# Kernel optimization log

Measured on AMD Instinct MI355X. Metric: run time of the kernel, lower is better.

The kernel has to match this reference:

```python
import jax, jax.numpy as jnp
import numpy as np

MROPE_SECTION = [16, 24, 24]
HEAD_DIM = 128
NUM_HEADS = 16
NUM_KV_HEADS = 8
EPS = 1e-6


def rmsnorm(x, w, eps=EPS):
    xf = x.astype(jnp.float32)
    var = jnp.mean(xf * xf, axis=-1, keepdims=True)
    return (w * (xf * jax.lax.rsqrt(var + eps))).astype(x.dtype)


def rotate_half(x):
    d = x.shape[-1] // 2
    return jnp.concatenate([-x[..., d:], x[..., :d]], axis=-1)


def build_mrope(c):
    # c: [3, B, S, head_dim]; pick modality i%3 per section (non-interleaved path)
    sec = MROPE_SECTION * 2
    splits = np.cumsum(sec)[:-1]
    parts = jnp.split(c, splits, axis=-1)
    out = jnp.concatenate([p[i % 3] for i, p in enumerate(parts)], axis=-1)  # [B,S,hd]
    return out[:, None]  # unsqueeze dim 1 -> [B,1,S,hd]


def setup_inputs() -> dict:
    key = jax.random.key(0)
    ks = jax.random.split(key, 8)
    B, S, D = 2, 2048, 2048
    hd, H, KV = HEAD_DIM, NUM_HEADS, NUM_KV_HEADS
    hidden_states = jax.random.normal(ks[0], (B, S, D), jnp.float32)
    cos = jax.random.uniform(ks[1], (3, B, S, hd), jnp.float32, -1.0, 1.0)
    sin = jax.random.uniform(ks[2], (3, B, S, hd), jnp.float32, -1.0, 1.0)
    # additive causal mask [B,1,S,S]
    neg = jnp.full((S, S), -1e9, jnp.float32)
    causal = jnp.triu(neg, k=1)
    attention_mask = jnp.broadcast_to(causal[None, None], (B, 1, S, S))
    sc = 0.02
    Wq = jax.random.normal(ks[3], (D, H * hd), jnp.float32) * sc
    Wk = jax.random.normal(ks[4], (D, KV * hd), jnp.float32) * sc
    Wv = jax.random.normal(ks[5], (D, KV * hd), jnp.float32) * sc
    Wo = jax.random.normal(ks[6], (H * hd, D), jnp.float32) * sc
    q_norm_w = jnp.ones((hd,), jnp.float32)
    k_norm_w = jnp.ones((hd,), jnp.float32)
    return dict(hidden_states=hidden_states, cos=cos, sin=sin,
                attention_mask=attention_mask, Wq=Wq, Wk=Wk, Wv=Wv, Wo=Wo,
                q_norm_w=q_norm_w, k_norm_w=k_norm_w)


def reference(hidden_states, cos, sin, attention_mask, Wq, Wk, Wv, Wo, q_norm_w, k_norm_w):
    B, S, D = hidden_states.shape
    hd, H, KV = HEAD_DIM, NUM_HEADS, NUM_KV_HEADS
    groups = H // KV
    scaling = hd ** -0.5

    q = (hidden_states @ Wq).reshape(B, S, H, hd)
    k = (hidden_states @ Wk).reshape(B, S, KV, hd)
    v = (hidden_states @ Wv).reshape(B, S, KV, hd)

    q = rmsnorm(q, q_norm_w).transpose(0, 2, 1, 3)  # [B,H,S,hd]
    k = rmsnorm(k, k_norm_w).transpose(0, 2, 1, 3)  # [B,KV,S,hd]
    v = v.transpose(0, 2, 1, 3)                      # [B,KV,S,hd]

    c = build_mrope(cos)  # [B,1,S,hd]
    s = build_mrope(sin)
    q = q * c + rotate_half(q) * s
    k = k * c + rotate_half(k) * s

    # repeat_kv (GQA)
    k = jnp.repeat(k, groups, axis=1)  # [B,H,S,hd]
    v = jnp.repeat(v, groups, axis=1)

    scores = jnp.einsum('bhqd,bhkd->bhqk', q, k) * scaling + attention_mask
    attn = jax.nn.softmax(scores.astype(jnp.float32), axis=-1).astype(q.dtype)
    out = jnp.einsum('bhqk,bhkd->bqhd', attn, v).reshape(B, S, H * hd)
    return out @ Wo
```

## Files before the change

### kernel.cpp

```cpp
#include <hip/hip_runtime.h>
#include <hip/hip_bf16.h>

typedef unsigned short u16;
typedef __bf16 bf16x8 __attribute__((ext_vector_type(8)));
typedef float f32x4 __attribute__((ext_vector_type(4)));

#define B_ 2
#define S_ 2048
#define SCALE_LOG2E 0.12751743f

static __device__ __forceinline__ u16 f2bf(float f) {
    union { float f; unsigned int u; } v; v.f = f;
    unsigned int r = v.u + 0x7fffu + ((v.u >> 16) & 1u);
    return (u16)(r >> 16);
}
static __device__ __forceinline__ float bf2f(unsigned int u) {
    union { unsigned int u; float f; } v; v.u = u << 16;
    return v.f;
}

__device__ __forceinline__ void gload16(const u16* g, u16* l) {
    __builtin_amdgcn_global_load_lds(
        (const __attribute__((address_space(1))) u16*)g,
        (__attribute__((address_space(3))) u16*)l,
        16, 0, 0);
}

__global__ __launch_bounds__(256) void prep(
    const float* __restrict__ hs, u16* __restrict__ hsb,
    const float* __restrict__ Wq, const float* __restrict__ Wk,
    const float* __restrict__ Wv, const float* __restrict__ Wo,
    u16* __restrict__ wqkvb, u16* __restrict__ wob)
{
    __shared__ float tile[32][33];
    int z = blockIdx.x;
    if (z < 8192) {
        int i = z * 256 + threadIdx.x;
        float4 v = reinterpret_cast<const float4*>(hs)[i];
        ushort4 o;
        o.x = f2bf(v.x); o.y = f2bf(v.y); o.z = f2bf(v.z); o.w = f2bf(v.w);
        reinterpret_cast<ushort4*>(hsb)[i] = o;
        return;
    }
    z -= 8192;
    const float* src; u16* dst; int srs, ct, zz;
    if (z < 4096)      { src = Wq; dst = wqkvb;               srs = 2048; ct = 64; zz = z; }
    else if (z < 6144) { src = Wk; dst = wqkvb + 2048 * 2048; srs = 1024; ct = 32; zz = z - 4096; }
    else if (z < 8192) { src = Wv; dst = wqkvb + 3072 * 2048; srs = 1024; ct = 32; zz = z - 6144; }
    else               { src = Wo; dst = wob;                 srs = 2048; ct = 64; zz = z - 8192; }
    int c0 = (zz % ct) << 5, r0 = (zz / ct) << 5;
    int t = threadIdx.x, tx = t & 7, ty = t >> 3;
    float4 v = *(const float4*)&src[(size_t)(r0 + ty) * srs + c0 + 4 * tx];
    tile[ty][4 * tx + 0] = v.x; tile[ty][4 * tx + 1] = v.y;
    tile[ty][4 * tx + 2] = v.z; tile[ty][4 * tx + 3] = v.w;
    __syncthreads();
    ushort4 o;
    o.x = f2bf(tile[4 * tx + 0][ty]); o.y = f2bf(tile[4 * tx + 1][ty]);
    o.z = f2bf(tile[4 * tx + 2][ty]); o.w = f2bf(tile[4 * tx + 3][ty]);
    *(ushort4*)&dst[(size_t)(c0 + ty) * 2048 + r0 + 4 * tx] = o;
}

template<int BM, int BN, int OBF>
__global__ __launch_bounds__(256, 2) void gemm_tile(
    const u16* __restrict__ A, const u16* __restrict__ Bt,
    void* __restrict__ Cv, int M, int N, int K)
{
    constexpr int RM = BM / 32;
    constexpr int RN = BN / 32;
    constexpr int NGA = BM / 64;
    constexpr int NGB = BN / 64;
    __shared__ __align__(16) u16 As[2][BM * 32];
    __shared__ __align__(16) u16 Bs[2][BN * 32];
    int t = threadIdx.x;
    int wave = t >> 6, lane = t & 63;
    int quad = lane >> 4, l16 = lane & 15;
    int wm = (wave >> 1) * (BM / 2), wn = (wave & 1) * (BN / 2);
    int m0 = blockIdx.y * BM, n0 = blockIdx.x * BN;

    f32x4 acc[RM][RN];
#pragma unroll
    for (int i = 0; i < RM; ++i)
#pragma unroll
        for (int j = 0; j < RN; ++j)
            acc[i][j] = (f32x4){0.f, 0.f, 0.f, 0.f};

    int srow = wave * 16 + (lane >> 2);
    int sc8 = (lane & 3) << 3;
    const u16* Ap = A + (size_t)(m0 + srow) * K + sc8;
    const u16* Bp = Bt + (size_t)(n0 + srow) * K + sc8;
    size_t row64 = (size_t)64 * K;
    int lofs = (wave * 16) * 32;

#pragma unroll
    for (int g = 0; g < NGA; ++g) gload16(Ap + g * row64, &As[0][lofs + g * 64 * 32]);
#pragma unroll
    for (int g = 0; g < NGB; ++g) gload16(Bp + g * row64, &Bs[0][lofs + g * 64 * 32]);

    int it = 0;
    for (int k0 = 0; k0 < K; k0 += 32, ++it) {
        int buf = it & 1;
        __syncthreads();
        if (k0 + 32 < K) {
            u16* dA = &As[buf ^ 1][lofs];
            u16* dB = &Bs[buf ^ 1][lofs];
#pragma unroll
            for (int g = 0; g < NGA; ++g) gload16(Ap + g * row64 + k0 + 32, dA + g * 64 * 32);
#pragma unroll
            for (int g = 0; g < NGB; ++g) gload16(Bp + g * row64 + k0 + 32, dB + g * 64 * 32);
        }
        bf16x8 af[RM], bfr[RN];
#pragma unroll
        for (int i = 0; i < RM; ++i)
            af[i] = *(const bf16x8*)(&As[buf][(wm + i * 16 + l16) * 32 + quad * 8]);
#pragma unroll
        for (int j = 0; j < RN; ++j)
            bfr[j] = *(const bf16x8*)(&Bs[buf][(wn + j * 16 + l16) * 32 + quad * 8]);
#pragma unroll
        for (int i = 0; i < RM; ++i)
#pragma unroll
            for (int j = 0; j < RN; ++j)
                acc[i][j] = __builtin_amdgcn_mfma_f32_16x16x32_bf16(af[i], bfr[j], acc[i][j], 0, 0, 0);
    }

    if (OBF) {
        u16* C16 = (u16*)Cv;
#pragma unroll
        for (int i = 0; i < RM; ++i) {
            int rbase = m0 + wm + i * 16 + quad * 4;
#pragma unroll
            for (int j = 0; j < RN; ++j) {
                int col = n0 + wn + j * 16 + l16;
#pragma unroll
                for (int r = 0; r < 4; ++r)
                    C16[(size_t)(rbase + r) * N + col] = f2bf(acc[i][j][r]);
            }
        }
    } else {
        float* Cf = (float*)Cv;
#pragma unroll
        for (int i = 0; i < RM; ++i) {
            int rbase = m0 + wm + i * 16 + quad * 4;
#pragma unroll
            for (int j = 0; j < RN; ++j) {
                int col = n0 + wn + j * 16 + l16;
#pragma unroll
                for (int r = 0; r < 4; ++r)
                    Cf[(size_t)(rbase + r) * N + col] = acc[i][j][r];
            }
        }
    }
}

__global__ __launch_bounds__(256) void post(
    const u16* __restrict__ qkvb, const float* __restrict__ cosb,
    const float* __restrict__ sinb, const float* __restrict__ qw,
    const float* __restrict__ kw, u16* __restrict__ qout, u16* __restrict__ kout,
    u16* __restrict__ vbo)
{
    __shared__ u16 tile[32][36];
    int zb = blockIdx.x;
    if (zb < 24576) {
        int row = zb & 4095;
        int b = row >> 11, s = row & 2047;
        int wave = threadIdx.x >> 6, lane = threadIdx.x & 63;
        int hv = (zb >> 12) * 4 + wave;
        bool isq = hv < 16;
        int h = isq ? hv : hv - 16;
        const u16* src = qkvb + (size_t)row * 4096 + (isq ? h * 128 : 2048 + h * 128);
        int d0 = lane << 1;
        unsigned int xu = *(const unsigned int*)(src + d0);
        float x0 = bf2f(xu & 0xffffu), x1 = bf2f(xu >> 16);
        float ss = x0 * x0 + x1 * x1;
#pragma unroll
        for (int off = 32; off >= 1; off >>= 1) ss += __shfl_xor(ss, off);
        float rstd = rsqrtf(ss * (1.0f / 128.0f) + 1e-6f);
        const float* w = isq ? qw : kw;
        float2 wv = *(const float2*)(w + d0);
        float xn0 = x0 * rstd * wv.x;
        float xn1 = x1 * rstd * wv.y;
        float p0 = __shfl_xor(xn0, 32);
        float p1 = __shfl_xor(xn1, 32);
        float rh0 = (lane < 32) ? -p0 : p0;
        float rh1 = (lane < 32) ? -p1 : p1;
        int md = d0 < 16 ? 0 : d0 < 40 ? 1 : d0 < 64 ? 2 : d0 < 80 ? 0 : d0 < 104 ? 1 : 2;
        size_t cidx = ((size_t)md * (B_ * S_) + row) * 128 + d0;
        float2 c  = *(const float2*)(cosb + cidx);
        float2 sn = *(const float2*)(sinb + cidx);
        float fs = isq ? SCALE_LOG2E : 1.0f;
        float o0 = (xn0 * c.x + rh0 * sn.x) * fs;
        float o1 = (xn1 * c.y + rh1 * sn.y) * fs;
        size_t orow = isq ? ((size_t)(b * 16 + h) * 2048 + s) * 128
                          : ((size_t)(b * 8 + h) * 2048 + s) * 128;
        unsigned int pack = (unsigned int)f2bf(o0) | ((unsigned int)f2bf(o1) << 16);
        u16* dst = isq ? qout : kout;
        *(unsigned int*)(dst + orow + d0) = pack;
        return;
    }
    int z2 = zb - 24576;
    int bxi = z2 & 3, byi = (z2 >> 2) & 63, zz = z2 >> 8;
    const u16* s = qkvb + (size_t)(zz >> 3) * 2048 * 4096 + 3072 + (zz & 7) * 128;
    u16* d = vbo + (size_t)zz * 128 * 2048;
    int c0 = bxi << 5, r0 = byi << 5;
    int t = threadIdx.x, tx = t & 7, ty = t >> 3;
    ushort4 v = *(const ushort4*)&s[(size_t)(r0 + ty) * 4096 + c0 + 4 * tx];
    tile[ty][4 * tx + 0] = v.x; tile[ty][4 * tx + 1] = v.y;
    tile[ty][4 * tx + 2] = v.z; tile[ty][4 * tx + 3] = v.w;
    __syncthreads();
    ushort4 o;
    o.x = tile[4 * tx + 0][ty]; o.y = tile[4 * tx + 1][ty];
    o.z = tile[4 * tx + 2][ty]; o.w = tile[4 * tx + 3][ty];
    *(ushort4*)&d[(size_t)(c0 + ty) * 2048 + r0 + 4 * tx] = o;
}

__global__ __launch_bounds__(256, 2) void attention(
    const u16* __restrict__ qb, const u16* __restrict__ kb,
    const u16* __restrict__ vt, u16* __restrict__ ao)
{
    __shared__ __align__(16) u16 Ks[2][64 * 128];
    __shared__ __align__(16) u16 Vs[2][128 * 64];
    __shared__ __align__(16) __bf16 Ps[4][2][16 * 64];

    int t = threadIdx.x;
    int wave = t >> 6, lane = t & 63;
    int quad = lane >> 4, l16 = lane & 15;
    int bx = blockIdx.x;
    int hi = bx >> 8, u = bx & 255;
    int q5 = u & 31;
    int qt = hi ? q5 : 31 - q5;
    int bkv = ((u >> 5) << 1) | hi;
    int b = bkv >> 3, kvh = bkv & 7;
    int q0 = qt << 6;

    bf16x8 af_q[2][4];
#pragma unroll
    for (int hh = 0; hh < 2; ++hh) {
        const u16* qsrc = qb + ((size_t)(b * 16 + kvh * 2 + hh) * 2048 + q0 + wave * 16 + l16) * 128 + quad * 8;
#pragma unroll
        for (int ks = 0; ks < 4; ++ks)
            af_q[hh][ks] = *(const bf16x8*)(qsrc + ks * 32);
    }

    const u16* kbase = kb + (size_t)bkv * 2048 * 128;
    const u16* vbase = vt + (size_t)bkv * 128 * 2048;
    const u16* kg[4]; const u16* vg[4];
    u16* kl0[4]; u16* kl1[4]; u16* vl0[4]; u16* vl1[4];
    {
        int kc = lane & 15, vc = lane & 7;
#pragma unroll
        for (int j = 0; j < 4; ++j) {
            int kr = wave * 16 + j * 4 + (lane >> 4);
            kg[j] = kbase + (size_t)kr * 128 + ((kc ^ (kr & 15)) << 3);
            int vr = wave * 32 + j * 8 + (lane >> 3);
            vg[j] = vbase + (size_t)vr * 2048 + ((vc ^ (vr & 7)) << 3);
            kl0[j] = &Ks[0][(wave * 16 + j * 4) * 128];
            kl1[j] = &Ks[1][(wave * 16 + j * 4) * 128];
            vl0[j] = &Vs[0][(wave * 32 + j * 8) * 64];
            vl1[j] = &Vs[1][(wave * 32 + j * 8) * 64];
        }
    }

    f32x4 o_acc[2][8];
    float lsum[2][4];
#pragma unroll
    for (int hh = 0; hh < 2; ++hh) {
#pragma unroll
        for (int i = 0; i < 8; ++i) o_acc[hh][i] = (f32x4){0.f, 0.f, 0.f, 0.f};
#pragma unroll
        for (int r = 0; r < 4; ++r) lsum[hh][r] = 0.f;
    }

#pragma unroll
    for (int j = 0; j < 4; ++j) { gload16(kg[j], kl0[j]); gload16(vg[j], vl0[j]); }

    for (int kt = 0; kt <= qt; ++kt) {
        int buf = kt & 1;
        __syncthreads();
        if (kt < qt) {
            size_t ko = (size_t)(kt + 1) * 64 * 128;
            int vo = (kt + 1) * 64;
            if (buf) {
#pragma unroll
                for (int j = 0; j < 4; ++j) { gload16(kg[j] + ko, kl0[j]); gload16(vg[j] + vo, vl0[j]); }
            } else {
#pragma unroll
                for (int j = 0; j < 4; ++j) { gload16(kg[j] + ko, kl1[j]); gload16(vg[j] + vo, vl1[j]); }
            }
        }
        const u16* Kb = Ks[buf];
        const u16* Vb = Vs[buf];

        f32x4 sa[2][4];
#pragma unroll
        for (int nt = 0; nt < 4; ++nt) { sa[0][nt] = (f32x4){0.f,0.f,0.f,0.f}; sa[1][nt] = (f32x4){0.f,0.f,0.f,0.f}; }
#pragma unroll
        for (int nt = 0; nt < 4; ++nt)
#pragma unroll
            for (int ks = 0; ks < 4; ++ks) {
                bf16x8 bk = *(const bf16x8*)(&Kb[(nt * 16 + l16) * 128 + ((((ks << 2) | quad) ^ l16) << 3)]);
                sa[0][nt] = __builtin_amdgcn_mfma_f32_16x16x32_bf16(af_q[0][ks], bk, sa[0][nt], 0, 0, 0);
                sa[1][nt] = __builtin_amdgcn_mfma_f32_16x16x32_bf16(af_q[1][ks], bk, sa[1][nt], 0, 0, 0);
            }

        bool diag = (kt == qt);
#pragma unroll
        for (int hh = 0; hh < 2; ++hh)
#pragma unroll
            for (int r = 0; r < 4; ++r) {
                int row = quad * 4 + r;
                int qi = wave * 16 + row;
#pragma unroll
                for (int nt = 0; nt < 4; ++nt) {
                    float pe = __builtin_amdgcn_exp2f(sa[hh][nt][r]);
                    int col = nt * 16 + l16;
                    if (diag && col > qi) pe = 0.f;
                    lsum[hh][r] += pe;
                    Ps[wave][hh][row * 64 + (col ^ ((row & 7) << 3))] = (__bf16)pe;
                }
            }

#pragma unroll
        for (int ks = 0; ks < 2; ++ks) {
            int csw = (((ks << 2) | quad) ^ (l16 & 7)) << 3;
            bf16x8 pa0 = *(const bf16x8*)(&Ps[wave][0][l16 * 64 + csw]);
            bf16x8 pa1 = *(const bf16x8*)(&Ps[wave][1][l16 * 64 + csw]);
#pragma unroll
            for (int dt = 0; dt < 8; ++dt) {
                bf16x8 vf = *(const bf16x8*)(&Vb[(dt * 16 + l16) * 64 + csw]);
                o_acc[0][dt] = __builtin_amdgcn_mfma_f32_16x16x32_bf16(pa0, vf, o_acc[0][dt], 0, 0, 0);
                o_acc[1][dt] = __builtin_amdgcn_mfma_f32_16x16x32_bf16(pa1, vf, o_acc[1][dt], 0, 0, 0);
            }
        }
    }

#pragma unroll
    for (int hh = 0; hh < 2; ++hh) {
#pragma unroll
        for (int r = 0; r < 4; ++r)
#pragma unroll
            for (int off = 1; off < 16; off <<= 1) lsum[hh][r] += __shfl_xor(lsum[hh][r], off);
        size_t obase = (((size_t)b * 2048 + q0 + wave * 16) * 16 + (kvh * 2 + hh)) * 128;
#pragma unroll
        for (int r = 0; r < 4; ++r) {
            float inv = 1.0f / lsum[hh][r];
            int qrow = quad * 4 + r;
#pragma unroll
            for (int dt = 0; dt < 8; ++dt)
                ao[obase + (size_t)qrow * 2048 + dt * 16 + l16] = f2bf(o_acc[hh][dt][r] * inv);
        }
    }
}

extern "C" void kernel_launch(void* const* d_in, const int* in_sizes, int n_in,
                              void* d_out, int out_size, void* d_ws, size_t ws_size,
                              hipStream_t stream) {
    const float* hs   = (const float*)d_in[0];
    const float* cosb = (const float*)d_in[1];
    const float* sinb = (const float*)d_in[2];
    const float* Wq = (const float*)d_in[4];
    const float* Wk = (const float*)d_in[5];
    const float* Wv = (const float*)d_in[6];
    const float* Wo = (const float*)d_in[7];
    const float* qw = (const float*)d_in[8];
    const float* kw = (const float*)d_in[9];
    float* out = (float*)d_out;

    char* ws = (char*)d_ws;
    u16* hsb   = (u16*)(ws);
    u16* wqkvb = (u16*)(ws + 16777216);
    u16* wob   = (u16*)(ws + 33554432);
    u16* qkvb  = (u16*)(ws + 41943040);
    u16* qb    = (u16*)(ws + 75497472);
    u16* kb    = (u16*)(ws + 92274688);
    u16* vb    = (u16*)(ws + 100663296);
    u16* aob   = (u16*)(ws + 109051904);

    prep<<<20480, 256, 0, stream>>>(hs, hsb, Wq, Wk, Wv, Wo, wqkvb, wob);

    gemm_tile<128, 128, 1><<<dim3(32, 32), 256, 0, stream>>>(hsb, wqkvb, qkvb, 4096, 4096, 2048);

    post<<<28672, 256, 0, stream>>>(qkvb, cosb, sinb, qw, kw, qb, kb, vb);

    attention<<<512, 256, 0, stream>>>(qb, kb, vb, aob);

    gemm_tile<128, 128, 0><<<dim3(16, 32), 256, 0, stream>>>(aob, wob, out, 4096, 2048, 2048);
}
```

Before: 373.0 us.

## Add 256x256 pipelined GEMM kernel with XOR-swizzled LDS for QKV projection

Replaces the 128x128 tiled GEMM for the QKV projection with a new 512-thread kernel using 256x256 tiles. It double-buffers A and B in LDS with direct global-to-LDS loads and interleaves the loads with MFMA phases using explicit barriers, waitcnts and setprio. It also XOR-swizzles the LDS layout against bank conflicts and remaps block IDs for cache locality. The goal is more data reuse per tile and overlap of memory traffic with matrix math, at the cost of heavy register pressure and fragile hand-written synchronization.

```diff
diff --git a/kernel.cpp b/kernel.cpp
--- a/kernel.cpp
+++ b/kernel.cpp
@@ -25,6 +25,12 @@
         (__attribute__((address_space(3))) u16*)l,
         16, 0, 0);
 }
+
+#define BAR()  asm volatile("s_barrier" ::: "memory")
+#define WL0()  asm volatile("s_waitcnt lgkmcnt(0)" ::: "memory")
+#define WL8()  asm volatile("s_waitcnt lgkmcnt(8)" ::: "memory")
+#define WVM4() asm volatile("s_waitcnt vmcnt(4)" ::: "memory")
+#define WVM0() asm volatile("s_waitcnt vmcnt(0)" ::: "memory")
 
 __global__ __launch_bounds__(256) void prep(
     const float* __restrict__ hs, u16* __restrict__ hsb,
@@ -58,6 +64,149 @@
     o.x = f2bf(tile[4 * tx + 0][ty]); o.y = f2bf(tile[4 * tx + 1][ty]);
     o.z = f2bf(tile[4 * tx + 2][ty]); o.w = f2bf(tile[4 * tx + 3][ty]);
     *(ushort4*)&dst[(size_t)(c0 + ty) * 2048 + r0 + 4 * tx] = o;
+}
+
+__device__ __forceinline__ void ldA2(bf16x8 (&aq)[2][2], const u16* bufp, int rbase, int quad) {
+#pragma unroll
+    for (int mm = 0; mm < 2; ++mm) {
+        int r = rbase + mm * 16;
+#pragma unroll
+        for (int ks = 0; ks < 2; ++ks)
+            aq[mm][ks] = *(const bf16x8*)(bufp + r * 64 + ((((ks << 2) | quad) ^ (r & 7)) << 3));
+    }
+}
+__device__ __forceinline__ void ldB4(bf16x8 (&bq)[4][2], const u16* bufp, int rbase, int quad) {
+#pragma unroll
+    for (int n = 0; n < 4; ++n) {
+        int r = rbase + n * 16;
+#pragma unroll
+        for (int ks = 0; ks < 2; ++ks)
+            bq[n][ks] = *(const bf16x8*)(bufp + r * 64 + ((((ks << 2) | quad) ^ (r & 7)) << 3));
+    }
+}
+__device__ __forceinline__ void mfma16(f32x4 (&acc)[8][4], const bf16x8 (&aq)[2][2],
+                                       const bf16x8 (&bq)[4][2], int p) {
+    __builtin_amdgcn_s_setprio(1);
+#pragma unroll
+    for (int n = 0; n < 4; ++n) {
+#pragma unroll
+        for (int mm = 0; mm < 2; ++mm) {
+            acc[2 * p + mm][n] = __builtin_amdgcn_mfma_f32_16x16x32_bf16(aq[mm][0], bq[n][0], acc[2 * p + mm][n], 0, 0, 0);
+            acc[2 * p + mm][n] = __builtin_amdgcn_mfma_f32_16x16x32_bf16(aq[mm][1], bq[n][1], acc[2 * p + mm][n], 0, 0, 0);
+        }
+    }
+    __builtin_amdgcn_s_setprio(0);
+}
+
+__global__ __launch_bounds__(512, 2) void gemm256(
+    const u16* __restrict__ A, const u16* __restrict__ Bt,
+    u16* __restrict__ C, int M, int N, int K)
+{
+    __shared__ __align__(16) u16 As[2][16384];
+    __shared__ __align__(16) u16 Bs[2][16384];
+
+    int nbx = N >> 8;
+    int bid = blockIdx.x, nwg = gridDim.x;
+    int swz = (bid & 7) * (nwg >> 3) + (bid >> 3);
+    int by = swz / nbx, bx = swz - by * nbx;
+    int m0 = by << 8, n0 = bx << 8;
+
+    int t = threadIdx.x;
+    int wave = t >> 6, lane = t & 63;
+    int quad = lane >> 4, l16 = lane & 15;
+    int wr = wave >> 2, wc = wave & 3;
+
+    int srow = wave * 8 + (lane >> 3);
+    int sgr  = (lane & 7) ^ (lane >> 3);
+    const u16* Ab = A  + (size_t)(m0 + srow) * K + sgr * 8;
+    const u16* Bb = Bt + (size_t)(n0 + srow) * K + sgr * 8;
+    size_t r64 = (size_t)64 * K;
+
+#define STG(Ld, Gp, H, KO) do { \
+    gload16((Gp) + (size_t)(2 * (H))     * r64 + (KO), &(Ld)[((H) * 128 +      wave * 8) * 64]); \
+    gload16((Gp) + (size_t)(2 * (H) + 1) * r64 + (KO), &(Ld)[((H) * 128 + 64 + wave * 8) * 64]); \
+} while (0)
+
+    f32x4 acc[8][4];
+#pragma unroll
+    for (int i = 0; i < 8; ++i)
+#pragma unroll
+        for (int j = 0; j < 4; ++j) acc[i][j] = (f32x4){0.f, 0.f, 0.f, 0.f};
+
+    STG(As[0], Ab, 0, 0); STG(As[0], Ab, 1, 0);
+    STG(Bs[0], Bb, 0, 0); STG(Bs[0], Bb, 1, 0);
+    STG(Bs[1], Bb, 0, 64); STG(Bs[1], Bb, 1, 64);
+    WVM4(); BAR();
+
+    int NT = K >> 6;
+    int arb = wr * 128 + l16;
+    int brb = wc * 64 + l16;
+    for (int U = 0; U < NT; U += 2) {
+        int kU = U << 6;
+        bool sf = (U + 2 < NT);
+        bf16x8 aq[2][2], bq[4][2];
+
+        ldB4(bq, Bs[0], brb, quad);
+        ldA2(aq, As[0], arb, quad);
+        STG(As[1], Ab, 0, kU + 64);
+        WL8();
+        BAR(); WL0(); __builtin_amdgcn_sched_barrier(0);
+        mfma16(acc, aq, bq, 0);
+        BAR();
+        ldA2(aq, As[0], arb + 32, quad);
+        STG(As[1], Ab, 1, kU + 64);
+        BAR(); WL0(); __builtin_amdgcn_sched_barrier(0);
+        mfma16(acc, aq, bq, 1);
+        BAR();
+        ldA2(aq, As[0], arb + 64, quad);
+        if (sf) STG(Bs[0], Bb, 0, kU + 128);
+        BAR(); WL0(); __builtin_amdgcn_sched_barrier(0);
+        mfma16(acc, aq, bq, 2);
+        BAR();
+        ldA2(aq, As[0], arb + 96, quad);
+        if (sf) STG(Bs[0], Bb, 1, kU + 128);
+        BAR(); WL0(); __builtin_amdgcn_sched_barrier(0);
+        mfma16(acc, aq, bq, 3);
+        if (sf) WVM4(); else WVM0();
+        BAR();
+
+        ldB4(bq, Bs[1], brb, quad);
+        ldA2(aq, As[1], arb, quad);
+        if (sf) STG(As[0], Ab, 0, kU + 128);
+        WL8();
+        BAR(); WL0(); __builtin_amdgcn_sched_barrier(0);
+        mfma16(acc, aq, bq, 0);
+        BAR();
+        ldA2(aq, As[1], arb + 32, quad);
+        if (sf) STG(As[0], Ab, 1, kU + 128);
+        BAR(); WL0(); __builtin_amdgcn_sched_barrier(0);
+        mfma16(acc, aq, bq, 1);
+        BAR();
+        ldA2(aq, As[1], arb + 64, quad);
+        if (sf) STG(Bs[1], Bb, 0, kU + 192);
+        BAR(); WL0(); __builtin_amdgcn_sched_barrier(0);
+        mfma16(acc, aq, bq, 2);
+        BAR();
+        ldA2(aq, As[1], arb + 96, quad);
+        if (sf) STG(Bs[1], Bb, 1, kU + 192);
+        BAR(); WL0(); __builtin_amdgcn_sched_barrier(0);
+        mfma16(acc, aq, bq, 3);
+        if (sf) WVM4();
+        BAR();
+    }
+#undef STG
+
+#pragma unroll
+    for (int m = 0; m < 8; ++m) {
+        int rbase = m0 + wr * 128 + m * 16 + quad * 4;
+#pragma unroll
+        for (int n = 0; n < 4; ++n) {
+            int col = n0 + wc * 64 + n * 16 + l16;
+#pragma unroll
+            for (int r = 0; r < 4; ++r)
+                C[(size_t)(rbase + r) * N + col] = f2bf(acc[m][n][r]);
+        }
+    }
 }
 
 template<int BM, int BN, int OBF>
@@ -376,7 +525,7 @@
 
     prep<<<20480, 256, 0, stream>>>(hs, hsb, Wq, Wk, Wv, Wo, wqkvb, wob);
 
-    gemm_tile<128, 128, 1><<<dim3(32, 32), 256, 0, stream>>>(hsb, wqkvb, qkvb, 4096, 4096, 2048);
+    gemm256<<<256, 512, 0, stream>>>(hsb, wqkvb, qkvb, 4096, 4096, 2048);
 
     post<<<28672, 256, 0, stream>>>(qkvb, cosb, sinb, qw, kw, qb, kb, vb);
 
```

Result: faster. 355.4 us (-4.7%).
